# Kernel tuning notes

Hardware: AMD Instinct MI355X
Metric: run time of the kernel (lower is better)

## Reference

```python
import jax, jax.numpy as jnp
import numpy as np

BN_EPS = 1e-5


def setup_inputs() -> dict:
    key = jax.random.key(0)
    ks = jax.random.split(key, 8)
    N, C, T, V, M = 32, 64, 300, 25, 2
    O, S = 64, 3  # out_channels, num_subset
    x = jax.random.normal(ks[0], (N, C, T, V, M), jnp.float32)
    PA = jax.random.normal(ks[1], (S, V, V), jnp.float32) * 0.1
    conv_w = jax.random.normal(ks[2], (O * S, C), jnp.float32) * (1.0 / np.sqrt(C))
    conv_b = jax.random.normal(ks[3], (O * S,), jnp.float32) * 0.01
    bn_gamma = jnp.ones((O,), jnp.float32)
    bn_beta = jnp.zeros((O,), jnp.float32)
    bn_mean = jax.random.normal(ks[4], (O,), jnp.float32) * 0.1
    bn_var = jax.random.uniform(ks[5], (O,), jnp.float32, 0.5, 1.5)
    return {"x": x, "PA": PA, "conv_w": conv_w, "conv_b": conv_b,
            "bn_gamma": bn_gamma, "bn_beta": bn_beta,
            "bn_mean": bn_mean, "bn_var": bn_var}


def reference(x, PA, conv_w, conv_b, bn_gamma, bn_beta, bn_mean, bn_var):
    N, C, T, V, M = x.shape
    S = PA.shape[0]
    O = conv_w.shape[0] // S
    # (N, C, T, V, M) -> (N*M, C, T, V)
    xb = jnp.transpose(x, (0, 4, 1, 2, 3)).reshape(N * M, C, T, V)
    res = xb  # identity residual (in_channels == out_channels, stride == 1)
    # 1x1 conv == per-position matmul over channels
    y = jnp.einsum('bctv,oc->botv', xb, conv_w) + conv_b[None, :, None, None]
    y = y.reshape(N * M, S, O, T, V)
    # sum over subsets of per-subset adjacency mixes (fused einsum)
    z = jnp.einsum('bsctv,svw->bctw', y, PA)
    # BatchNorm2d (inference form with running stats)
    scale = bn_gamma / jnp.sqrt(bn_var + BN_EPS)
    z = z * scale[None, :, None, None] + (bn_beta - bn_mean * scale)[None, :, None, None]
    z = jax.nn.relu(z)
    out = jax.nn.relu(z + res)
    # (N*M, O, T, V) -> (N, O, T, V, M)
    return jnp.transpose(out.reshape(N, M, O, T, V), (0, 2, 3, 4, 1))
```

## Files before the change

kernel.cpp:

```cpp
#include <hip/hip_runtime.h>
#include <cstddef>
#include <cstdint>

#define N_  32
#define C_  64
#define T_  300
#define V_  25
#define M_  2
#define S_  3
#define O_  64
#define OS_ 192
#define TB  6
#define NT_BLK (T_/TB)
#define CTVM (C_*T_*V_*M_)
#define TVM  (T_*V_*M_)
#define VM   (V_*M_)
#define XPITCH 72
#define YPITCH 72

typedef short  short8  __attribute__((ext_vector_type(8)));
typedef float  float4_ __attribute__((ext_vector_type(4)));

__device__ __forceinline__ short f2bf(float f) {
    uint32_t u = __float_as_uint(f);
    u += 0x7FFFu + ((u >> 16) & 1u);
    return (short)(u >> 16);
}
__device__ __forceinline__ unsigned pk2bf(float a, float b) {
    const uint32_t ua = (uint32_t)(uint16_t)f2bf(a);
    const uint32_t ub = (uint32_t)(uint16_t)f2bf(b);
    return ua | (ub << 16);
}

__global__ void stgcn_prep(const float* __restrict__ Wc, const float* __restrict__ PA,
                           const float* __restrict__ g,  const float* __restrict__ b,
                           const float* __restrict__ mn, const float* __restrict__ vr,
                           short* __restrict__ Wb, short* __restrict__ PAb,
                           float* __restrict__ scl, float* __restrict__ sft)
{
    const int i = blockIdx.x * 256 + threadIdx.x;
    if (i < OS_ * C_) Wb[i] = f2bf(Wc[i]);
    const int r = i - OS_ * C_;
    if (r >= 0 && r < S_ * 32 * 32) {
        const int s = r >> 10, rem = r & 1023, wp = rem >> 5, vp = rem & 31;
        const float val = (wp < V_ && vp < V_) ? PA[s * V_ * V_ + vp * V_ + wp] : 0.0f;
        PAb[r] = f2bf(val);
    }
    const int q = r - S_ * 32 * 32;
    if (q >= 0 && q < O_) {
        const float sc = g[q] * rsqrtf(vr[q] + 1e-5f);
        scl[q] = sc;
        sft[q] = b[q] - mn[q] * sc;
    }
}

__global__ __launch_bounds__(256, 3)
void stgcn_main(const float* __restrict__ x, const float* __restrict__ cb,
                const short* __restrict__ Wb, const short* __restrict__ PAb,
                const float* __restrict__ sclg, const float* __restrict__ sftg,
                float* __restrict__ out)
{
    __shared__ short Xb[2][64 * XPITCH];
    __shared__ short Ys[OS_ * YPITCH];
    __shared__ float sclS[O_], sftS[O_];

    const int tid  = threadIdx.x;
    const int wv   = tid >> 6;
    const int lane = tid & 63;
    const int quad = lane >> 4;
    const int l15  = lane & 15;

    const int n  = blockIdx.x / NT_BLK;
    const int t0 = (blockIdx.x % NT_BLK) * TB;
    const size_t xbase = (size_t)n * CTVM;

    for (int i = tid; i < 2 * 14 * XPITCH; i += 256) {
        const int bf = i / (14 * XPITCH);
        const int r  = i - bf * (14 * XPITCH);
        const int pr = r / XPITCH, cc = r - pr * XPITCH;
        const int pos = (pr < 7) ? (25 + pr) : (50 + pr);
        Xb[bf][pos * XPITCH + cc] = 0;
    }
    if (tid < O_) { sclS[tid] = sclg[tid]; sftS[tid] = sftg[tid]; }

    const int wbase = wv * 48;
    short8 aW[3][2];
    #pragma unroll
    for (int mt = 0; mt < 3; ++mt)
        #pragma unroll
        for (int ks = 0; ks < 2; ++ks)
            aW[mt][ks] = *(const short8*)(Wb + (wbase + mt * 16 + l15) * C_ + ks * 32 + quad * 8);

    const int m2 = wv >> 1, hh = wv & 1;
    short8 bP[3];
    #pragma unroll
    for (int s = 0; s < 3; ++s)
        bP[s] = *(const short8*)(PAb + (s * 1024 + (hh * 16 + l15) * 32 + quad * 8));

    float cbw[3];
    #pragma unroll
    for (int mt = 0; mt < 3; ++mt) cbw[mt] = cb[wbase + mt * 16 + l15];

    {
        const float* xt = x + xbase + (size_t)t0 * VM;
        #pragma unroll
        for (int k = 0; k < 4; ++k) {
            const int p = tid + k * 256;
            if (p < 800) {
                const int v = p % 25, cp = p / 25;
                const float2 f0 = *(const float2*)(xt + (size_t)(2 * cp)     * TVM + v * 2);
                const float2 f1 = *(const float2*)(xt + (size_t)(2 * cp + 1) * TVM + v * 2);
                ((unsigned*)Xb[0])[v * 36 + cp]        = pk2bf(f0.x, f1.x);
                ((unsigned*)Xb[0])[(32 + v) * 36 + cp] = pk2bf(f0.y, f1.y);
            }
        }
    }

    int cur = 0;
    for (int tt = 0; tt < TB; ++tt) {
        __syncthreads();

        float2 R0[4], R1[4];
        const bool pf = (tt + 1 < TB);
        if (pf) {
            const float* xt = x + xbase + (size_t)(t0 + tt + 1) * VM;
            #pragma unroll
            for (int k = 0; k < 4; ++k) {
                const int p = tid + k * 256;
                if (p < 800) {
                    const int v = p % 25, cp = p / 25;
                    R0[k] = *(const float2*)(xt + (size_t)(2 * cp)     * TVM + v * 2);
                    R1[k] = *(const float2*)(xt + (size_t)(2 * cp + 1) * TVM + v * 2);
                }
            }
        }

        const short* Xc = Xb[cur];
        short8 bX[4][2];
        #pragma unroll
        for (int nt = 0; nt < 4; ++nt)
            #pragma unroll
            for (int ks = 0; ks < 2; ++ks)
                bX[nt][ks] = *(const short8*)(Xc + (nt * 16 + l15) * XPITCH + ks * 32 + quad * 8);

        #pragma unroll
        for (int mt = 0; mt < 3; ++mt) {
            #pragma unroll
            for (int nt = 0; nt < 4; ++nt) {
                float4_ acc = { cbw[mt], cbw[mt], cbw[mt], cbw[mt] };
                acc = __builtin_amdgcn_mfma_f32_16x16x32_bf16(bX[nt][0], aW[mt][0], acc, 0, 0, 0);
                acc = __builtin_amdgcn_mfma_f32_16x16x32_bf16(bX[nt][1], aW[mt][1], acc, 0, 0, 0);
                const int os = wbase + mt * 16 + l15;
                *(uint2*)(Ys + os * YPITCH + nt * 16 + quad * 4) =
                    make_uint2(pk2bf(acc[0], acc[1]), pk2bf(acc[2], acc[3]));
            }
        }
        __syncthreads();

        float4_ z[4];
        #pragma unroll
        for (int ot = 0; ot < 4; ++ot) { z[ot][0]=0.f; z[ot][1]=0.f; z[ot][2]=0.f; z[ot][3]=0.f; }
        #pragma unroll
        for (int s = 0; s < 3; ++s) {
            #pragma unroll
            for (int ot = 0; ot < 4; ++ot) {
                const short8 aY = *(const short8*)(Ys + (s * 64 + ot * 16 + l15) * YPITCH + m2 * 32 + quad * 8);
                z[ot] = __builtin_amdgcn_mfma_f32_16x16x32_bf16(aY, bP[s], z[ot], 0, 0, 0);
            }
        }

        const int wc = hh * 16 + l15;
        const int t  = t0 + tt;
        if (wc < V_) {
            const int xrow = (m2 * 32 + wc) * XPITCH;
            #pragma unroll
            for (int ot = 0; ot < 4; ++ot) {
                #pragma unroll
                for (int r = 0; r < 4; ++r) {
                    const int o = ot * 16 + quad * 4 + r;
                    const float res = __uint_as_float(((unsigned)(unsigned short)Xc[xrow + o]) << 16);
                    float q = fmaf(z[ot][r], sclS[o], sftS[o]);
                    q = fmaxf(q, 0.0f);
                    q = fmaxf(q + res, 0.0f);
                    out[xbase + (size_t)o * TVM + (size_t)t * VM + wc * 2 + m2] = q;
                }
            }
        }

        if (pf) {
            short* Xn = Xb[cur ^ 1];
            #pragma unroll
            for (int k = 0; k < 4; ++k) {
                const int p = tid + k * 256;
                if (p < 800) {
                    const int v = p % 25, cp = p / 25;
                    ((unsigned*)Xn)[v * 36 + cp]        = pk2bf(R0[k].x, R1[k].x);
                    ((unsigned*)Xn)[(32 + v) * 36 + cp] = pk2bf(R0[k].y, R1[k].y);
                }
            }
        }
        cur ^= 1;
    }
}

extern "C" void kernel_launch(void* const* d_in, const int* in_sizes, int n_in,
                              void* d_out, int out_size, void* d_ws, size_t ws_size,
                              hipStream_t stream)
{
    const float* x    = (const float*)d_in[0];
    const float* PA   = (const float*)d_in[1];
    const float* Wc   = (const float*)d_in[2];
    const float* cb   = (const float*)d_in[3];
    const float* bn_g = (const float*)d_in[4];
    const float* bn_b = (const float*)d_in[5];
    const float* bn_m = (const float*)d_in[6];
    const float* bn_v = (const float*)d_in[7];
    float* out = (float*)d_out;

    char* ws = (char*)d_ws;
    short* Wb  = (short*)ws;
    short* PAb = (short*)(ws + 24576);
    float* scl = (float*)(ws + 30720);
    float* sft = (float*)(ws + 30976);

    stgcn_prep<<<61, 256, 0, stream>>>(Wc, PA, bn_g, bn_b, bn_m, bn_v, Wb, PAb, scl, sft);
    stgcn_main<<<N_ * NT_BLK, 256, 0, stream>>>(x, cb, Wb, PAb, scl, sft, out);
}
```

Measured before the change: 287.9 us.

## Single-buffer X tile, remap second-stage waves to emit float2 (m-pair) stores

Drops the double-buffered X tile in shared memory and reads the residual values into registers before the buffer is overwritten by the prefetch. The second-stage MFMA work is remapped so each wave covers two output-channel tiles for both persons, which lets each output write be a float2 store of the interleaved M pair instead of two scalar strided stores. Occupancy in launch bounds rises from 3 to 4 blocks per CU thanks to the smaller LDS footprint. This trades register pressure for residuals and the new tiling against fewer store instructions and higher occupancy.

New measurement: 342.3 us. 1.19x slower.

```diff
diff --git a/kernel.cpp b/kernel.cpp
--- a/kernel.cpp
+++ b/kernel.cpp
@@ -20,6 +20,7 @@
 
 typedef short  short8  __attribute__((ext_vector_type(8)));
 typedef float  float4_ __attribute__((ext_vector_type(4)));
+typedef unsigned short ushort4_ __attribute__((ext_vector_type(4)));
 
 __device__ __forceinline__ short f2bf(float f) {
     uint32_t u = __float_as_uint(f);
@@ -30,6 +31,9 @@
     const uint32_t ua = (uint32_t)(uint16_t)f2bf(a);
     const uint32_t ub = (uint32_t)(uint16_t)f2bf(b);
     return ua | (ub << 16);
+}
+__device__ __forceinline__ float bf2f(unsigned short u) {
+    return __uint_as_float(((unsigned)u) << 16);
 }
 
 __global__ void stgcn_prep(const float* __restrict__ Wc, const float* __restrict__ PA,
@@ -54,13 +58,13 @@
     }
 }
 
-__global__ __launch_bounds__(256, 3)
+__global__ __launch_bounds__(256, 4)
 void stgcn_main(const float* __restrict__ x, const float* __restrict__ cb,
                 const short* __restrict__ Wb, const short* __restrict__ PAb,
                 const float* __restrict__ sclg, const float* __restrict__ sftg,
                 float* __restrict__ out)
 {
-    __shared__ short Xb[2][64 * XPITCH];
+    __shared__ short Xb[64 * XPITCH];
     __shared__ short Ys[OS_ * YPITCH];
     __shared__ float sclS[O_], sftS[O_];
 
@@ -74,12 +78,10 @@
     const int t0 = (blockIdx.x % NT_BLK) * TB;
     const size_t xbase = (size_t)n * CTVM;
 
-    for (int i = tid; i < 2 * 14 * XPITCH; i += 256) {
-        const int bf = i / (14 * XPITCH);
-        const int r  = i - bf * (14 * XPITCH);
-        const int pr = r / XPITCH, cc = r - pr * XPITCH;
+    for (int i = tid; i < 14 * XPITCH; i += 256) {
+        const int pr = i / XPITCH, cc = i - pr * XPITCH;
         const int pos = (pr < 7) ? (25 + pr) : (50 + pr);
-        Xb[bf][pos * XPITCH + cc] = 0;
+        Xb[pos * XPITCH + cc] = 0;
     }
     if (tid < O_) { sclS[tid] = sclg[tid]; sftS[tid] = sftg[tid]; }
 
@@ -91,15 +93,16 @@
         for (int ks = 0; ks < 2; ++ks)
             aW[mt][ks] = *(const short8*)(Wb + (wbase + mt * 16 + l15) * C_ + ks * 32 + quad * 8);
 
-    const int m2 = wv >> 1, hh = wv & 1;
+    float cbw[3];
+    #pragma unroll
+    for (int mt = 0; mt < 3; ++mt) cbw[mt] = cb[wbase + mt * 16 + l15];
+
+    const int oh = wv >> 1, hh = wv & 1;
+    const int wc = hh * 16 + l15;
     short8 bP[3];
     #pragma unroll
     for (int s = 0; s < 3; ++s)
-        bP[s] = *(const short8*)(PAb + (s * 1024 + (hh * 16 + l15) * 32 + quad * 8));
-
-    float cbw[3];
-    #pragma unroll
-    for (int mt = 0; mt < 3; ++mt) cbw[mt] = cb[wbase + mt * 16 + l15];
+        bP[s] = *(const short8*)(PAb + s * 1024 + wc * 32 + quad * 8);
 
     {
         const float* xt = x + xbase + (size_t)t0 * VM;
@@ -110,13 +113,12 @@
                 const int v = p % 25, cp = p / 25;
                 const float2 f0 = *(const float2*)(xt + (size_t)(2 * cp)     * TVM + v * 2);
                 const float2 f1 = *(const float2*)(xt + (size_t)(2 * cp + 1) * TVM + v * 2);
-                ((unsigned*)Xb[0])[v * 36 + cp]        = pk2bf(f0.x, f1.x);
-                ((unsigned*)Xb[0])[(32 + v) * 36 + cp] = pk2bf(f0.y, f1.y);
-            }
-        }
-    }
-
-    int cur = 0;
+                ((unsigned*)Xb)[v * 36 + cp]        = pk2bf(f0.x, f1.x);
+                ((unsigned*)Xb)[(32 + v) * 36 + cp] = pk2bf(f0.y, f1.y);
+            }
+        }
+    }
+
     for (int tt = 0; tt < TB; ++tt) {
         __syncthreads();
 
@@ -135,13 +137,19 @@
             }
         }
 
-        const short* Xc = Xb[cur];
         short8 bX[4][2];
         #pragma unroll
         for (int nt = 0; nt < 4; ++nt)
             #pragma unroll
             for (int ks = 0; ks < 2; ++ks)
-                bX[nt][ks] = *(const short8*)(Xc + (nt * 16 + l15) * XPITCH + ks * 32 + quad * 8);
+                bX[nt][ks] = *(const short8*)(Xb + (nt * 16 + l15) * XPITCH + ks * 32 + quad * 8);
+
+        ushort4_ res[2][2];
+        #pragma unroll
+        for (int otl = 0; otl < 2; ++otl)
+            #pragma unroll
+            for (int m = 0; m < 2; ++m)
+                res[otl][m] = *(const ushort4_*)(Xb + (m * 32 + wc) * XPITCH + (oh * 2 + otl) * 16 + quad * 4);
 
         #pragma unroll
         for (int mt = 0; mt < 3; ++mt) {
@@ -157,49 +165,54 @@
         }
         __syncthreads();
 
-        float4_ z[4];
-        #pragma unroll
-        for (int ot = 0; ot < 4; ++ot) { z[ot][0]=0.f; z[ot][1]=0.f; z[ot][2]=0.f; z[ot][3]=0.f; }
+        float4_ z[2][2];
+        #pragma unroll
+        for (int otl = 0; otl < 2; ++otl)
+            #pragma unroll
+            for (int m = 0; m < 2; ++m) { z[otl][m][0]=0.f; z[otl][m][1]=0.f; z[otl][m][2]=0.f; z[otl][m][3]=0.f; }
         #pragma unroll
         for (int s = 0; s < 3; ++s) {
             #pragma unroll
-            for (int ot = 0; ot < 4; ++ot) {
-                const short8 aY = *(const short8*)(Ys + (s * 64 + ot * 16 + l15) * YPITCH + m2 * 32 + quad * 8);
-                z[ot] = __builtin_amdgcn_mfma_f32_16x16x32_bf16(aY, bP[s], z[ot], 0, 0, 0);
-            }
-        }
-
-        const int wc = hh * 16 + l15;
-        const int t  = t0 + tt;
-        if (wc < V_) {
-            const int xrow = (m2 * 32 + wc) * XPITCH;
-            #pragma unroll
-            for (int ot = 0; ot < 4; ++ot) {
+            for (int otl = 0; otl < 2; ++otl) {
                 #pragma unroll
-                for (int r = 0; r < 4; ++r) {
-                    const int o = ot * 16 + quad * 4 + r;
-                    const float res = __uint_as_float(((unsigned)(unsigned short)Xc[xrow + o]) << 16);
-                    float q = fmaf(z[ot][r], sclS[o], sftS[o]);
-                    q = fmaxf(q, 0.0f);
-                    q = fmaxf(q + res, 0.0f);
-                    out[xbase + (size_t)o * TVM + (size_t)t * VM + wc * 2 + m2] = q;
+                for (int m = 0; m < 2; ++m) {
+                    const short8 aY = *(const short8*)(Ys + (s * 64 + (oh * 2 + otl) * 16 + l15) * YPITCH + m * 32 + quad * 8);
+                    z[otl][m] = __builtin_amdgcn_mfma_f32_16x16x32_bf16(aY, bP[s], z[otl][m], 0, 0, 0);
                 }
             }
         }
 
         if (pf) {
-            short* Xn = Xb[cur ^ 1];
             #pragma unroll
             for (int k = 0; k < 4; ++k) {
                 const int p = tid + k * 256;
                 if (p < 800) {
                     const int v = p % 25, cp = p / 25;
-                    ((unsigned*)Xn)[v * 36 + cp]        = pk2bf(R0[k].x, R1[k].x);
-                    ((unsigned*)Xn)[(32 + v) * 36 + cp] = pk2bf(R0[k].y, R1[k].y);
-                }
-            }
-        }
-        cur ^= 1;
+                    ((unsigned*)Xb)[v * 36 + cp]        = pk2bf(R0[k].x, R1[k].x);
+                    ((unsigned*)Xb)[(32 + v) * 36 + cp] = pk2bf(R0[k].y, R1[k].y);
+                }
+            }
+        }
+
+        const int t = t0 + tt;
+        if (wc < V_) {
+            #pragma unroll
+            for (int otl = 0; otl < 2; ++otl) {
+                #pragma unroll
+                for (int r = 0; r < 4; ++r) {
+                    const int o = (oh * 2 + otl) * 16 + quad * 4 + r;
+                    const float sc = sclS[o], sh = sftS[o];
+                    float q0 = fmaf(z[otl][0][r], sc, sh);
+                    q0 = fmaxf(q0, 0.0f);
+                    q0 = fmaxf(q0 + bf2f((unsigned short)res[otl][0][r]), 0.0f);
+                    float q1 = fmaf(z[otl][1][r], sc, sh);
+                    q1 = fmaxf(q1, 0.0f);
+                    q1 = fmaxf(q1 + bf2f((unsigned short)res[otl][1][r]), 0.0f);
+                    *(float2*)(out + xbase + (size_t)o * TVM + (size_t)t * VM + wc * 2) =
+                        make_float2(q0, q1);
+                }
+            }
+        }
     }
 }
 
```

## Repartition waves by output channel to drop block barrier between GEMM stages

Applied to the files above, without the earlier changes.

Each wave now owns 16 output channels across all three subsets, so the adjacency-mix stage consumes only that wave's own conv results. Those results go through a per-wave scratch buffer in shared memory, and the second __syncthreads becomes an lgkmcnt wait. The residual is loaded as vector reads, both M values are written with a single float2 store, and bf16 packing uses v_perm. The cost is more PA fragments held in registers, and correctness now relies on the scratch buffer being written and read only within one wave.

After: 277.9 us. 3.5% less time.

```diff
diff --git a/kernel.cpp b/kernel.cpp
--- a/kernel.cpp
+++ b/kernel.cpp
@@ -16,10 +16,10 @@
 #define TVM  (T_*V_*M_)
 #define VM   (V_*M_)
 #define XPITCH 72
-#define YPITCH 72
 
 typedef short  short8  __attribute__((ext_vector_type(8)));
 typedef float  float4_ __attribute__((ext_vector_type(4)));
+typedef unsigned short ushort4_ __attribute__((ext_vector_type(4)));
 
 __device__ __forceinline__ short f2bf(float f) {
     uint32_t u = __float_as_uint(f);
@@ -27,9 +27,13 @@
     return (short)(u >> 16);
 }
 __device__ __forceinline__ unsigned pk2bf(float a, float b) {
-    const uint32_t ua = (uint32_t)(uint16_t)f2bf(a);
-    const uint32_t ub = (uint32_t)(uint16_t)f2bf(b);
-    return ua | (ub << 16);
+    unsigned ua = __float_as_uint(a), ub = __float_as_uint(b);
+    ua += 0x7FFFu + ((ua >> 16) & 1u);
+    ub += 0x7FFFu + ((ub >> 16) & 1u);
+    return __builtin_amdgcn_perm(ub, ua, 0x07060302u);
+}
+__device__ __forceinline__ float bf2f(unsigned short u) {
+    return __uint_as_float(((unsigned)u) << 16);
 }
 
 __global__ void stgcn_prep(const float* __restrict__ Wc, const float* __restrict__ PA,
@@ -61,7 +65,7 @@
                 float* __restrict__ out)
 {
     __shared__ short Xb[2][64 * XPITCH];
-    __shared__ short Ys[OS_ * YPITCH];
+    __shared__ uint2 scr[4 * 12 * 64];
     __shared__ float sclS[O_], sftS[O_];
 
     const int tid  = threadIdx.x;
@@ -83,23 +87,24 @@
     }
     if (tid < O_) { sclS[tid] = sclg[tid]; sftS[tid] = sftg[tid]; }
 
-    const int wbase = wv * 48;
+    const int osb = wv * 16;
     short8 aW[3][2];
     #pragma unroll
-    for (int mt = 0; mt < 3; ++mt)
+    for (int s = 0; s < 3; ++s)
         #pragma unroll
         for (int ks = 0; ks < 2; ++ks)
-            aW[mt][ks] = *(const short8*)(Wb + (wbase + mt * 16 + l15) * C_ + ks * 32 + quad * 8);
-
-    const int m2 = wv >> 1, hh = wv & 1;
-    short8 bP[3];
+            aW[s][ks] = *(const short8*)(Wb + (s * 64 + osb + l15) * C_ + ks * 32 + quad * 8);
+
+    float cbw[3];
+    #pragma unroll
+    for (int s = 0; s < 3; ++s) cbw[s] = cb[s * 64 + osb + l15];
+
+    short8 bPf[3][2];
     #pragma unroll
     for (int s = 0; s < 3; ++s)
-        bP[s] = *(const short8*)(PAb + (s * 1024 + (hh * 16 + l15) * 32 + quad * 8));
-
-    float cbw[3];
-    #pragma unroll
-    for (int mt = 0; mt < 3; ++mt) cbw[mt] = cb[wbase + mt * 16 + l15];
+        #pragma unroll
+        for (int wh = 0; wh < 2; ++wh)
+            bPf[s][wh] = *(const short8*)(PAb + s * 1024 + (wh * 16 + l15) * 32 + quad * 8);
 
     {
         const float* xt = x + xbase + (size_t)t0 * VM;
@@ -143,46 +148,66 @@
             for (int ks = 0; ks < 2; ++ks)
                 bX[nt][ks] = *(const short8*)(Xc + (nt * 16 + l15) * XPITCH + ks * 32 + quad * 8);
 
-        #pragma unroll
-        for (int mt = 0; mt < 3; ++mt) {
+        ushort4_ res[2][2];
+        #pragma unroll
+        for (int m = 0; m < 2; ++m)
+            #pragma unroll
+            for (int wh = 0; wh < 2; ++wh)
+                res[m][wh] = *(const ushort4_*)(Xc + (m * 32 + wh * 16 + l15) * XPITCH + osb + quad * 4);
+
+        #pragma unroll
+        for (int s = 0; s < 3; ++s) {
             #pragma unroll
             for (int nt = 0; nt < 4; ++nt) {
-                float4_ acc = { cbw[mt], cbw[mt], cbw[mt], cbw[mt] };
-                acc = __builtin_amdgcn_mfma_f32_16x16x32_bf16(bX[nt][0], aW[mt][0], acc, 0, 0, 0);
-                acc = __builtin_amdgcn_mfma_f32_16x16x32_bf16(bX[nt][1], aW[mt][1], acc, 0, 0, 0);
-                const int os = wbase + mt * 16 + l15;
-                *(uint2*)(Ys + os * YPITCH + nt * 16 + quad * 4) =
+                float4_ acc = { cbw[s], cbw[s], cbw[s], cbw[s] };
+                acc = __builtin_amdgcn_mfma_f32_16x16x32_bf16(bX[nt][0], aW[s][0], acc, 0, 0, 0);
+                acc = __builtin_amdgcn_mfma_f32_16x16x32_bf16(bX[nt][1], aW[s][1], acc, 0, 0, 0);
+                scr[wv * 768 + (s * 4 + nt) * 64 + lane] =
                     make_uint2(pk2bf(acc[0], acc[1]), pk2bf(acc[2], acc[3]));
             }
         }
-        __syncthreads();
-
-        float4_ z[4];
-        #pragma unroll
-        for (int ot = 0; ot < 4; ++ot) { z[ot][0]=0.f; z[ot][1]=0.f; z[ot][2]=0.f; z[ot][3]=0.f; }
+
+        asm volatile("s_waitcnt lgkmcnt(0)" ::: "memory");
+
+        float4_ z[2][2];
+        #pragma unroll
+        for (int m = 0; m < 2; ++m)
+            #pragma unroll
+            for (int wh = 0; wh < 2; ++wh) { z[m][wh][0]=0.f; z[m][wh][1]=0.f; z[m][wh][2]=0.f; z[m][wh][3]=0.f; }
+
+        const int lanepart = (((lane >> 4) & 1) * 32) + l15;
+        const int ntq      = (lane >> 5);
         #pragma unroll
         for (int s = 0; s < 3; ++s) {
             #pragma unroll
-            for (int ot = 0; ot < 4; ++ot) {
-                const short8 aY = *(const short8*)(Ys + (s * 64 + ot * 16 + l15) * YPITCH + m2 * 32 + quad * 8);
-                z[ot] = __builtin_amdgcn_mfma_f32_16x16x32_bf16(aY, bP[s], z[ot], 0, 0, 0);
-            }
-        }
-
-        const int wc = hh * 16 + l15;
-        const int t  = t0 + tt;
-        if (wc < V_) {
-            const int xrow = (m2 * 32 + wc) * XPITCH;
-            #pragma unroll
-            for (int ot = 0; ot < 4; ++ot) {
+            for (int m = 0; m < 2; ++m) {
+                union { short8 s8; uint2 u2[2]; } aY;
+                const int base = wv * 768 + (s * 4 + 2 * m + ntq) * 64;
+                aY.u2[0] = scr[base + lanepart];
+                aY.u2[1] = scr[base + lanepart + 16];
+                #pragma unroll
+                for (int wh = 0; wh < 2; ++wh)
+                    z[m][wh] = __builtin_amdgcn_mfma_f32_16x16x32_bf16(aY.s8, bPf[s][wh], z[m][wh], 0, 0, 0);
+            }
+        }
+
+        const int t = t0 + tt;
+        #pragma unroll
+        for (int wh = 0; wh < 2; ++wh) {
+            const int w = wh * 16 + l15;
+            if (w < V_) {
                 #pragma unroll
                 for (int r = 0; r < 4; ++r) {
-                    const int o = ot * 16 + quad * 4 + r;
-                    const float res = __uint_as_float(((unsigned)(unsigned short)Xc[xrow + o]) << 16);
-                    float q = fmaf(z[ot][r], sclS[o], sftS[o]);
-                    q = fmaxf(q, 0.0f);
-                    q = fmaxf(q + res, 0.0f);
-                    out[xbase + (size_t)o * TVM + (size_t)t * VM + wc * 2 + m2] = q;
+                    const int o = osb + quad * 4 + r;
+                    const float sc = sclS[o], sh = sftS[o];
+                    float q0 = fmaf(z[0][wh][r], sc, sh);
+                    q0 = fmaxf(q0, 0.0f);
+                    q0 = fmaxf(q0 + bf2f((unsigned short)res[0][wh][r]), 0.0f);
+                    float q1 = fmaf(z[1][wh][r], sc, sh);
+                    q1 = fmaxf(q1, 0.0f);
+                    q1 = fmaxf(q1 + bf2f((unsigned short)res[1][wh][r]), 0.0f);
+                    *(float2*)(out + xbase + (size_t)o * TVM + (size_t)t * VM + w * 2) =
+                        make_float2(q0, q1);
                 }
             }
         }
```
